# Kernel optimization log

Measured on AMD Instinct MI355X. Metric: run time of the kernel, lower is better.

The kernel has to match this reference:

```python
import jax, jax.numpy as jnp
import numpy as np

BATCH = 2
SEQ = 2048
D_MODEL = 512
D_STATE = 16
D_CONV = 4
D_INNER = 2 * D_MODEL  # expand=2


def setup_inputs() -> dict:
    key = jax.random.key(0)
    ks = jax.random.split(key, 7)
    s = 0.02
    x = jax.random.normal(ks[0], (BATCH, SEQ, D_MODEL), jnp.float32)
    W_in = jax.random.normal(ks[1], (2 * D_INNER, D_MODEL), jnp.float32) * s
    conv_w = jax.random.normal(ks[2], (D_INNER, 1, D_CONV), jnp.float32) * s  # depthwise kernel
    conv_b = jnp.zeros((D_INNER,), jnp.float32)
    W_x = jax.random.normal(ks[3], (2 * D_STATE, D_INNER), jnp.float32) * s
    W_dt = jax.random.normal(ks[4], (D_INNER, D_INNER), jnp.float32) * s
    b_dt = jnp.zeros((D_INNER,), jnp.float32)
    # A_log init: log of [1..d_state] broadcast over d_inner rows
    A_log = jnp.log(jnp.broadcast_to(jnp.arange(1, D_STATE + 1, dtype=jnp.float32), (D_INNER, D_STATE)))
    D_param = jnp.ones((D_INNER,), jnp.float32)
    W_out = jax.random.normal(ks[5], (D_MODEL, D_INNER), jnp.float32) * s
    return dict(x=x, W_in=W_in, conv_w=conv_w, conv_b=conv_b, W_x=W_x,
                W_dt=W_dt, b_dt=b_dt, A_log=A_log, D_param=D_param, W_out=W_out)


def reference(x, W_in, conv_w, conv_b, W_x, W_dt, b_dt, A_log, D_param, W_out):
    # in_proj, split into x-branch and gate z
    xz = x @ W_in.T                             # [B, L, 2*di]
    xi, z = jnp.split(xz, 2, axis=-1)
    # depthwise causal conv1d (torch pads both sides then slices [:seq_len] == left-pad only)
    h = jnp.transpose(xi, (0, 2, 1))            # [B, di, L]
    h = jax.lax.conv_general_dilated(
        h, conv_w, window_strides=(1,), padding=[(D_CONV - 1, 0)],
        dimension_numbers=('NCH', 'OIH', 'NCH'), feature_group_count=D_INNER)
    h = h + conv_b[None, :, None]
    h = jax.nn.silu(jnp.transpose(h, (0, 2, 1)))  # [B, L, di]

    A = -jnp.exp(A_log)                         # [di, ds]
    x_dbl = h @ W_x.T                           # [B, L, 2*ds]
    _delta_unused, Bmat = jnp.split(x_dbl, 2, axis=-1)  # B (also used as C): [B, L, ds]
    delta = jax.nn.softplus(h @ W_dt.T + b_dt)  # [B, L, di] (overwrites x_proj delta, as in source)

    def step(state, inp):
        d_t, B_t, h_t = inp                     # [B,di], [B,ds], [B,di]
        dA = jnp.exp(d_t[:, :, None] * A)       # [B, di, ds]
        state = dA * state + d_t[:, :, None] * B_t[:, None, :] * h_t[:, :, None]
        y_t = jnp.einsum('bds,bs->bd', state, B_t)  # C == B
        return state, y_t

    init = jnp.zeros((x.shape[0], D_INNER, D_STATE), x.dtype)
    _, ys = jax.lax.scan(step, init,
                         (jnp.swapaxes(delta, 0, 1), jnp.swapaxes(Bmat, 0, 1), jnp.swapaxes(h, 0, 1)))
    y = jnp.swapaxes(ys, 0, 1)                  # [B, L, di]
    y = (y + D_param * h) * jax.nn.silu(z)
    return y @ W_out.T                          # [B, L, d_model]
```

## Files before the change

### kernel.cpp

```cpp
#include <hip/hip_runtime.h>
#include <cstddef>
#include <cstdint>

#define NB 2
#define L_SEQ 2048
#define DM 512
#define DS 16
#define DI 1024
#define NC 64
#define CL (L_SEQ/NC)

typedef __attribute__((ext_vector_type(4))) float f32x4;
typedef __attribute__((ext_vector_type(8))) short bf16x8;

__device__ __forceinline__ float softplus_f(float x) {
  return (x > 20.f) ? x : log1pf(expf(x));
}
__device__ __forceinline__ float silu_f(float x) {
  return x / (1.f + expf(-x));
}
__device__ __forceinline__ ushort f2bf(float f) {
  uint32_t u = __float_as_uint(f);
  return (ushort)((u + 0x7fffu + ((u >> 16) & 1u)) >> 16);
}
__device__ __forceinline__ float bf2f(ushort h) {
  return __uint_as_float(((uint32_t)h) << 16);
}

__device__ __forceinline__ void gload16(const void* g, ushort* lds_wave_base) {
  __builtin_amdgcn_global_load_lds(
      (const __attribute__((address_space(1))) void*)g,
      (__attribute__((address_space(3))) void*)lds_wave_base, 16, 0, 0);
}

__global__ __launch_bounds__(256) void split_bf16(
    const float* __restrict__ in, ushort* __restrict__ hi,
    ushort* __restrict__ lo, int n4) {
  int i = blockIdx.x * 256 + threadIdx.x;
  if (i >= n4) return;
  float4 v = ((const float4*)in)[i];
  ushort h0 = f2bf(v.x), h1 = f2bf(v.y), h2 = f2bf(v.z), h3 = f2bf(v.w);
  ((ushort4*)hi)[i] = make_ushort4(h0, h1, h2, h3);
  ((ushort4*)lo)[i] = make_ushort4(
      f2bf(v.x - bf2f(h0)), f2bf(v.y - bf2f(h1)),
      f2bf(v.z - bf2f(h2)), f2bf(v.w - bf2f(h3)));
}

template <int ACT>
__global__ __launch_bounds__(512, 6) void gemm_mfma8(
    const ushort* __restrict__ Ahi, const ushort* __restrict__ Alo, int lda,
    const ushort* __restrict__ Bhi, const ushort* __restrict__ Blo, int ldb,
    const float* __restrict__ bias, float* __restrict__ C, int ldc,
    float* __restrict__ Bmout, int K) {
  constexpr int BM = 128, BN = 64;
  constexpr int AT = BM * 32;
  constexpr int BT = BN * 32;
  constexpr int BUF = 2 * AT + 2 * BT;
  constexpr int MR = 2, NR = 2;
  __shared__ __align__(16) ushort lds[2 * BUF];

  const int tid = threadIdx.x;
  const int lane = tid & 63;
  const int wave = tid >> 6;
  const int wr = wave >> 1;
  const int wc = wave & 1;

  const int nx = gridDim.x;
  const int nwg = nx * gridDim.y;
  int bid = blockIdx.y * nx + blockIdx.x;
  bid = (bid & 7) * (nwg >> 3) + (bid >> 3);
  const int m0 = (bid / nx) * BM;
  const int n0 = (bid % nx) * BN;

  const int ra = tid >> 2;
  const int kga = (tid & 3) ^ ((ra >> 1) & 3);
  const size_t aoff = (size_t)(m0 + ra) * lda + kga * 8;
  const int tq = tid & 255;
  const int rb = tq >> 2;
  const int kgb = (tq & 3) ^ ((rb >> 1) & 3);
  const size_t boff = (size_t)(n0 + rb) * ldb + kgb * 8;
  const ushort* Bsel = (wave < 4) ? Bhi : Blo;
  const int blds = 2 * AT + ((wave < 4) ? wave * 512 : BT + (wave - 4) * 512);

  const int fr = lane & 15, fq = lane >> 4;
  const int kswz = fq ^ ((fr >> 1) & 3);
  int aoffs[MR], boffs[NR];
#pragma unroll
  for (int m = 0; m < MR; m++) aoffs[m] = (wr * 32 + m * 16 + fr) * 32 + kswz * 8;
#pragma unroll
  for (int n = 0; n < NR; n++) boffs[n] = (wc * 32 + n * 16 + fr) * 32 + kswz * 8;

  f32x4 acc[MR][NR];
#pragma unroll
  for (int m = 0; m < MR; m++)
#pragma unroll
    for (int n = 0; n < NR; n++) acc[m][n] = (f32x4){0.f, 0.f, 0.f, 0.f};

  const int nsteps = K >> 5;

#define STAGE(base, kk)                                     \
  {                                                         \
    ushort* bp = (base);                                    \
    gload16(Ahi + aoff + (kk), bp + wave * 512);            \
    gload16(Alo + aoff + (kk), bp + AT + wave * 512);       \
    gload16(Bsel + boff + (kk), bp + blds);                 \
  }

#define COMPUTE(base)                                                          \
  {                                                                            \
    const ushort* cp = (base);                                                 \
    bf16x8 ah[MR], al[MR], bh[NR], bl[NR];                                     \
    _Pragma("unroll")                                                          \
    for (int m = 0; m < MR; m++) ah[m] = *(const bf16x8*)(cp + aoffs[m]);      \
    _Pragma("unroll")                                                          \
    for (int m = 0; m < MR; m++) al[m] = *(const bf16x8*)(cp + AT + aoffs[m]); \
    _Pragma("unroll")                                                          \
    for (int n = 0; n < NR; n++) bh[n] = *(const bf16x8*)(cp + 2 * AT + boffs[n]); \
    _Pragma("unroll")                                                          \
    for (int n = 0; n < NR; n++) bl[n] = *(const bf16x8*)(cp + 2 * AT + BT + boffs[n]); \
    _Pragma("unroll")                                                          \
    for (int m = 0; m < MR; m++)                                               \
      _Pragma("unroll")                                                        \
      for (int n = 0; n < NR; n++)                                             \
        acc[m][n] = __builtin_amdgcn_mfma_f32_16x16x32_bf16(ah[m], bh[n], acc[m][n], 0, 0, 0); \
    _Pragma("unroll")                                                          \
    for (int m = 0; m < MR; m++)                                               \
      _Pragma("unroll")                                                        \
      for (int n = 0; n < NR; n++)                                             \
        acc[m][n] = __builtin_amdgcn_mfma_f32_16x16x32_bf16(al[m], bh[n], acc[m][n], 0, 0, 0); \
    _Pragma("unroll")                                                          \
    for (int m = 0; m < MR; m++)                                               \
      _Pragma("unroll")                                                        \
      for (int n = 0; n < NR; n++)                                             \
        acc[m][n] = __builtin_amdgcn_mfma_f32_16x16x32_bf16(ah[m], bl[n], acc[m][n], 0, 0, 0); \
  }

  STAGE(lds, 0);
  __syncthreads();
  for (int t = 0; t < nsteps; ++t) {
    if (t + 1 < nsteps) STAGE(lds + ((t + 1) & 1) * BUF, (t + 1) << 5);
    COMPUTE(lds + (t & 1) * BUF);
    __syncthreads();
  }
#undef STAGE
#undef COMPUTE

#pragma unroll
  for (int m = 0; m < MR; m++) {
    const int row = m0 + wr * 32 + m * 16 + fq * 4;
#pragma unroll
    for (int n = 0; n < NR; n++) {
      const int col = n0 + wc * 32 + n * 16 + fr;
      if (ACT == 1) {
        if (col < DI) {
          const float bcol = bias[col];
#pragma unroll
          for (int j = 0; j < 4; j++)
            C[(size_t)(row + j) * ldc + col] = softplus_f(acc[m][n][j] + bcol);
        } else if (col < DI + DS) {
#pragma unroll
          for (int j = 0; j < 4; j++)
            Bmout[(size_t)(row + j) * DS + (col - DI)] = acc[m][n][j];
        }
      } else {
#pragma unroll
        for (int j = 0; j < 4; j++)
          C[(size_t)(row + j) * ldc + col] = acc[m][n][j];
      }
    }
  }
}

template <int ACT>
__global__ __launch_bounds__(256, 5) void gemm_mfma4(
    const ushort* __restrict__ Ahi, const ushort* __restrict__ Alo, int lda,
    const ushort* __restrict__ Bhi, const ushort* __restrict__ Blo, int ldb,
    const float* __restrict__ bias, float* __restrict__ C, int ldc, int K) {
  constexpr int BM = 64, BN = 64;
  constexpr int AT = BM * 32;
  constexpr int BT = BN * 32;
  constexpr int BUF = 2 * AT + 2 * BT;
  constexpr int MR = 2, NR = 2;
  __shared__ __align__(16) ushort lds[2 * BUF];

  const int tid = threadIdx.x;
  const int lane = tid & 63;
  const int wave = tid >> 6;
  const int wr = wave >> 1, wc = wave & 1;

  const int nx = gridDim.x;
  const int nwg = nx * gridDim.y;
  int bid = blockIdx.y * nx + blockIdx.x;
  bid = (bid & 7) * (nwg >> 3) + (bid >> 3);
  const int m0 = (bid / nx) * BM;
  const int n0 = (bid % nx) * BN;

  const int r0 = tid >> 2;
  const int kg = (tid & 3) ^ ((r0 >> 1) & 3);
  const size_t aoff0 = (size_t)(m0 + r0) * lda + kg * 8;
  const size_t boff0 = (size_t)(n0 + r0) * ldb + kg * 8;

  const int fr = lane & 15, fq = lane >> 4;
  const int kswz = fq ^ ((fr >> 1) & 3);
  int aoffs[MR], boffs[NR];
#pragma unroll
  for (int m = 0; m < MR; m++) aoffs[m] = (wr * 32 + m * 16 + fr) * 32 + kswz * 8;
#pragma unroll
  for (int n = 0; n < NR; n++) boffs[n] = (wc * 32 + n * 16 + fr) * 32 + kswz * 8;

  f32x4 acc[MR][NR];
#pragma unroll
  for (int m = 0; m < MR; m++)
#pragma unroll
    for (int n = 0; n < NR; n++) acc[m][n] = (f32x4){0.f, 0.f, 0.f, 0.f};

  const int nsteps = K >> 5;

#define STAGE(base, kk)                                           \
  {                                                               \
    ushort* bp = (base);                                          \
    gload16(Ahi + aoff0 + (kk), bp + wave * 512);                 \
    gload16(Alo + aoff0 + (kk), bp + AT + wave * 512);            \
    gload16(Bhi + boff0 + (kk), bp + 2 * AT + wave * 512);        \
    gload16(Blo + boff0 + (kk), bp + 2 * AT + BT + wave * 512);   \
  }

#define COMPUTE(base)                                                          \
  {                                                                            \
    const ushort* cp = (base);                                                 \
    bf16x8 ah[MR], al[MR], bh[NR], bl[NR];                                     \
    _Pragma("unroll")                                                          \
    for (int m = 0; m < MR; m++) ah[m] = *(const bf16x8*)(cp + aoffs[m]);      \
    _Pragma("unroll")                                                          \
    for (int m = 0; m < MR; m++) al[m] = *(const bf16x8*)(cp + AT + aoffs[m]); \
    _Pragma("unroll")                                                          \
    for (int n = 0; n < NR; n++) bh[n] = *(const bf16x8*)(cp + 2 * AT + boffs[n]); \
    _Pragma("unroll")                                                          \
    for (int n = 0; n < NR; n++) bl[n] = *(const bf16x8*)(cp + 2 * AT + BT + boffs[n]); \
    _Pragma("unroll")                                                          \
    for (int m = 0; m < MR; m++)                                               \
      _Pragma("unroll")                                                        \
      for (int n = 0; n < NR; n++)                                             \
        acc[m][n] = __builtin_amdgcn_mfma_f32_16x16x32_bf16(ah[m], bh[n], acc[m][n], 0, 0, 0); \
    _Pragma("unroll")                                                          \
    for (int m = 0; m < MR; m++)                                               \
      _Pragma("unroll")                                                        \
      for (int n = 0; n < NR; n++)                                             \
        acc[m][n] = __builtin_amdgcn_mfma_f32_16x16x32_bf16(al[m], bh[n], acc[m][n], 0, 0, 0); \
    _Pragma("unroll")                                                          \
    for (int m = 0; m < MR; m++)                                               \
      _Pragma("unroll")                                                        \
      for (int n = 0; n < NR; n++)                                             \
        acc[m][n] = __builtin_amdgcn_mfma_f32_16x16x32_bf16(ah[m], bl[n], acc[m][n], 0, 0, 0); \
  }

  STAGE(lds, 0);
  __syncthreads();
  for (int t = 0; t < nsteps; ++t) {
    if (t + 1 < nsteps) STAGE(lds + ((t + 1) & 1) * BUF, (t + 1) << 5);
    COMPUTE(lds + (t & 1) * BUF);
    __syncthreads();
  }
#undef STAGE
#undef COMPUTE

#pragma unroll
  for (int m = 0; m < MR; m++) {
    const int row = m0 + wr * 32 + m * 16 + fq * 4;
#pragma unroll
    for (int n = 0; n < NR; n++) {
      const int col = n0 + wc * 32 + n * 16 + fr;
      float bcol = (ACT == 1) ? bias[col] : 0.f;
#pragma unroll
      for (int j = 0; j < 4; j++) {
        float v = acc[m][n][j];
        if (ACT == 1) v = softplus_f(v + bcol);
        C[(size_t)(row + j) * ldc + col] = v;
      }
    }
  }
}

__global__ __launch_bounds__(256) void conv_silu_kernel(
    const float* __restrict__ xz, const float* __restrict__ conv_w,
    const float* __restrict__ conv_b, float* __restrict__ h,
    ushort* __restrict__ h_hi, ushort* __restrict__ h_lo) {
  const int idx = blockIdx.x * 256 + threadIdx.x;
  const int c = idx & (DI - 1);
  const int r = idx >> 10;
  const int l = r & (L_SEQ - 1);
  const float w0 = conv_w[c * 4 + 0];
  const float w1 = conv_w[c * 4 + 1];
  const float w2 = conv_w[c * 4 + 2];
  const float w3 = conv_w[c * 4 + 3];
  const float* xp = xz + (size_t)r * (2 * DI) + c;
  float acc = conv_b[c];
  if (l >= 3) acc += xp[-3 * 2 * DI] * w0;
  if (l >= 2) acc += xp[-2 * 2 * DI] * w1;
  if (l >= 1) acc += xp[-1 * 2 * DI] * w2;
  acc += xp[0] * w3;
  const float hv = silu_f(acc);
  h[idx] = hv;
  const ushort hh = f2bf(hv);
  h_hi[idx] = hh;
  h_lo[idx] = f2bf(hv - bf2f(hh));
}

__global__ __launch_bounds__(256) void scan_phase1(
    const float* __restrict__ delta, const float* __restrict__ h,
    const float* __restrict__ Bm, const float* __restrict__ A_log,
    float* __restrict__ aprod, float* __restrict__ blocal) {
  __shared__ float sB[CL * DS];
  const int tid = threadIdx.x;
  const int bid = blockIdx.x;
  const int cblk = bid & 3;
  const int chunk = (bid >> 2) & (NC - 1);
  const int b = bid >> 8;
  const int c = cblk * 256 + tid;
  const size_t row0 = (size_t)b * L_SEQ + chunk * CL;
  ((float2*)sB)[tid] = ((const float2*)(Bm + row0 * DS))[tid];
  __syncthreads();

  float Acs[DS], state[DS];
#pragma unroll
  for (int s = 0; s < DS; s += 4) {
    float4 al = *(const float4*)(A_log + (size_t)c * DS + s);
    Acs[s + 0] = -__expf(al.x);
    Acs[s + 1] = -__expf(al.y);
    Acs[s + 2] = -__expf(al.z);
    Acs[s + 3] = -__expf(al.w);
    state[s + 0] = 0.f; state[s + 1] = 0.f; state[s + 2] = 0.f; state[s + 3] = 0.f;
  }
  const float* dp = delta + row0 * DI + c;
  const float* hp = h + row0 * DI + c;
  float sdt = 0.f;
  for (int t = 0; t < CL; ++t) {
    const float dt = dp[(size_t)t * DI];
    const float ht = hp[(size_t)t * DI];
    const float dth = dt * ht;
    sdt += dt;
#pragma unroll
    for (int s = 0; s < DS; ++s)
      state[s] = __expf(dt * Acs[s]) * state[s] + dth * sB[t * DS + s];
  }
  const size_t o = (((size_t)b * NC + chunk) * DI + c) * DS;
#pragma unroll
  for (int s = 0; s < DS; s += 4) {
    *(float4*)(aprod + o + s) = make_float4(
        __expf(Acs[s] * sdt), __expf(Acs[s + 1] * sdt),
        __expf(Acs[s + 2] * sdt), __expf(Acs[s + 3] * sdt));
    *(float4*)(blocal + o + s) = make_float4(state[s], state[s + 1], state[s + 2], state[s + 3]);
  }
}

__global__ __launch_bounds__(256) void scan_phase2(
    float* __restrict__ aprod, const float* __restrict__ blocal) {
  const int idx = blockIdx.x * 256 + threadIdx.x;
  const int b = idx >> 14;
  const int cs = idx & 16383;
  float st = 0.f;
  for (int ch = 0; ch < NC; ++ch) {
    const size_t o = (size_t)(b * NC + ch) * (DI * DS) + cs;
    const float a = aprod[o];
    const float bl = blocal[o];
    aprod[o] = st;
    st = a * st + bl;
  }
}

__global__ __launch_bounds__(256) void scan_phase3(
    const float* __restrict__ delta, const float* __restrict__ h,
    const float* __restrict__ Bm, const float* __restrict__ A_log,
    const float* __restrict__ sinit, float* __restrict__ xz,
    const float* __restrict__ Dp) {
  __shared__ float sB[CL * DS];
  const int tid = threadIdx.x;
  const int bid = blockIdx.x;
  const int cblk = bid & 3;
  const int chunk = (bid >> 2) & (NC - 1);
  const int b = bid >> 8;
  const int c = cblk * 256 + tid;
  const size_t row0 = (size_t)b * L_SEQ + chunk * CL;
  ((float2*)sB)[tid] = ((const float2*)(Bm + row0 * DS))[tid];
  __syncthreads();

  float Acs[DS], state[DS];
  const size_t o = (((size_t)b * NC + chunk) * DI + c) * DS;
#pragma unroll
  for (int s = 0; s < DS; s += 4) {
    float4 al = *(const float4*)(A_log + (size_t)c * DS + s);
    Acs[s + 0] = -__expf(al.x);
    Acs[s + 1] = -__expf(al.y);
    Acs[s + 2] = -__expf(al.z);
    Acs[s + 3] = -__expf(al.w);
    float4 sv = *(const float4*)(sinit + o + s);
    state[s + 0] = sv.x; state[s + 1] = sv.y; state[s + 2] = sv.z; state[s + 3] = sv.w;
  }
  const float* dp = delta + row0 * DI + c;
  const float* hp = h + row0 * DI + c;
  const float* zp = xz + row0 * (2 * DI) + DI + c;
  ushort* yrow = (ushort*)(xz + row0 * (2 * DI)) + c;
  const float Dc = Dp[c];
  for (int t = 0; t < CL; ++t) {
    const float dt = dp[(size_t)t * DI];
    const float ht = hp[(size_t)t * DI];
    const float z = zp[(size_t)t * (2 * DI)];
    const float dth = dt * ht;
    float yv = 0.f;
#pragma unroll
    for (int s = 0; s < DS; ++s) {
      const float bt = sB[t * DS + s];
      state[s] = __expf(dt * Acs[s]) * state[s] + dth * bt;
      yv += state[s] * bt;
    }
    const float g = (yv + Dc * ht) * silu_f(z);
    const ushort gh = f2bf(g);
    yrow[(size_t)t * 4096] = gh;
    yrow[(size_t)t * 4096 + 1024] = f2bf(g - bf2f(gh));
  }
}

extern "C" void kernel_launch(void* const* d_in, const int* in_sizes, int n_in,
                              void* d_out, int out_size, void* d_ws, size_t ws_size,
                              hipStream_t stream) {
  const float* x      = (const float*)d_in[0];
  const float* W_in   = (const float*)d_in[1];
  const float* conv_w = (const float*)d_in[2];
  const float* conv_b = (const float*)d_in[3];
  const float* W_x    = (const float*)d_in[4];
  const float* W_dt   = (const float*)d_in[5];
  const float* b_dt   = (const float*)d_in[6];
  const float* A_log  = (const float*)d_in[7];
  const float* D_par  = (const float*)d_in[8];
  const float* W_out  = (const float*)d_in[9];
  float* out = (float*)d_out;

  const int rows = NB * L_SEQ;

  float* xz     = (float*)d_ws;
  float* h      = xz + (size_t)(8u << 20);
  float* delta  = h + (size_t)(4u << 20);
  float* Bm     = delta + (size_t)(4u << 20);
  ushort* W2hi  = (ushort*)(Bm + (size_t)(64u << 10));
  ushort* W2lo  = W2hi + (size_t)1088 * 1024;
  ushort* Wout_hi = W2lo + (size_t)1088 * 1024;
  ushort* Wout_lo = Wout_hi + (size_t)(512u << 10);
  float* xreg   = (float*)(Wout_lo + (size_t)(512u << 10));
  ushort* x_hi  = (ushort*)xreg;
  ushort* x_lo  = x_hi + (size_t)(2u << 20);
  ushort* Win_hi = x_lo + (size_t)(2u << 20);
  ushort* Win_lo = Win_hi + (size_t)(1u << 20);
  ushort* h_hi  = (ushort*)xreg;
  ushort* h_lo  = h_hi + (size_t)(4u << 20);
  float* aprod  = xreg;
  float* blocal = aprod + (size_t)(2u << 20);
  ushort* y_hi  = (ushort*)xz;
  ushort* y_lo  = y_hi + 1024;

  split_bf16<<<2048, 256, 0, stream>>>(x, x_hi, x_lo, rows * DM / 4);
  split_bf16<<<1024, 256, 0, stream>>>(W_in, Win_hi, Win_lo, 2 * DI * DM / 4);
  split_bf16<<<1024, 256, 0, stream>>>(W_dt, W2hi, W2lo, DI * DI / 4);
  split_bf16<<<16, 256, 0, stream>>>(W_x + DS * DI,
      W2hi + (size_t)DI * DI, W2lo + (size_t)DI * DI, DS * DI / 4);
  split_bf16<<<512, 256, 0, stream>>>(W_out, Wout_hi, Wout_lo, DM * DI / 4);

  gemm_mfma8<0><<<dim3(32, 32), 512, 0, stream>>>(
      x_hi, x_lo, DM, Win_hi, Win_lo, DM, nullptr, xz, 2 * DI, nullptr, DM);
  conv_silu_kernel<<<(rows * DI) / 256, 256, 0, stream>>>(xz, conv_w, conv_b, h, h_hi, h_lo);
  gemm_mfma8<1><<<dim3(17, 32), 512, 0, stream>>>(
      h_hi, h_lo, DI, W2hi, W2lo, DI, b_dt, delta, DI, Bm, DI);
  scan_phase1<<<NB * NC * (DI / 256), 256, 0, stream>>>(delta, h, Bm, A_log, aprod, blocal);
  scan_phase2<<<(NB * DI * DS) / 256, 256, 0, stream>>>(aprod, blocal);
  scan_phase3<<<NB * NC * (DI / 256), 256, 0, stream>>>(delta, h, Bm, A_log, aprod, xz, D_par);
  gemm_mfma4<0><<<dim3(8, 64), 256, 0, stream>>>(
      y_hi, y_lo, 4096, Wout_hi, Wout_lo, DI, nullptr, out, DM, DI);
}
```

Measured before the change: 208.6 us.

## Triple-buffer GEMM LDS pipeline with split barriers and fuse bf16 split launches

New measurement: 201.7 us. 3.3% less time.

```diff
diff --git a/kernel.cpp b/kernel.cpp
--- a/kernel.cpp
+++ b/kernel.cpp
@@ -33,21 +33,37 @@
       (__attribute__((address_space(3))) void*)lds_wave_base, 16, 0, 0);
 }
 
-__global__ __launch_bounds__(256) void split_bf16(
-    const float* __restrict__ in, ushort* __restrict__ hi,
-    ushort* __restrict__ lo, int n4) {
-  int i = blockIdx.x * 256 + threadIdx.x;
-  if (i >= n4) return;
+__device__ __forceinline__ void split4(const float4 v, ushort4* hi, ushort4* lo) {
+  ushort h0 = f2bf(v.x), h1 = f2bf(v.y), h2 = f2bf(v.z), h3 = f2bf(v.w);
+  *hi = make_ushort4(h0, h1, h2, h3);
+  *lo = make_ushort4(f2bf(v.x - bf2f(h0)), f2bf(v.y - bf2f(h1)),
+                     f2bf(v.z - bf2f(h2)), f2bf(v.w - bf2f(h3)));
+}
+
+__global__ __launch_bounds__(256) void split_all(
+    const float* __restrict__ x,    ushort* __restrict__ xh,  ushort* __restrict__ xl,
+    const float* __restrict__ win,  ushort* __restrict__ wih, ushort* __restrict__ wil,
+    const float* __restrict__ wdt,  ushort* __restrict__ wdh, ushort* __restrict__ wdl,
+    const float* __restrict__ wx,   ushort* __restrict__ wxh, ushort* __restrict__ wxl,
+    const float* __restrict__ wout, ushort* __restrict__ woh, ushort* __restrict__ wol) {
+  int bi = blockIdx.x;
+  const float* in; ushort* hi; ushort* lo; int i;
+  if (bi < 2048)      { in = x;    hi = xh;  lo = xl;  i = bi * 256 + threadIdx.x; }
+  else if (bi < 3072) { in = win;  hi = wih; lo = wil; i = (bi - 2048) * 256 + threadIdx.x; }
+  else if (bi < 4096) { in = wdt;  hi = wdh; lo = wdl; i = (bi - 3072) * 256 + threadIdx.x; }
+  else if (bi < 4112) { in = wx;   hi = wxh; lo = wxl; i = (bi - 4096) * 256 + threadIdx.x; }
+  else                { in = wout; hi = woh; lo = wol; i = (bi - 4112) * 256 + threadIdx.x; }
   float4 v = ((const float4*)in)[i];
-  ushort h0 = f2bf(v.x), h1 = f2bf(v.y), h2 = f2bf(v.z), h3 = f2bf(v.w);
-  ((ushort4*)hi)[i] = make_ushort4(h0, h1, h2, h3);
-  ((ushort4*)lo)[i] = make_ushort4(
-      f2bf(v.x - bf2f(h0)), f2bf(v.y - bf2f(h1)),
-      f2bf(v.z - bf2f(h2)), f2bf(v.w - bf2f(h3)));
-}
+  ushort4 h4, l4;
+  split4(v, &h4, &l4);
+  ((ushort4*)hi)[i] = h4;
+  ((ushort4*)lo)[i] = l4;
+}
+
+#define MFMA(a, b, c) __builtin_amdgcn_mfma_f32_16x16x32_bf16((a), (b), (c), 0, 0, 0)
 
 template <int ACT>
-__global__ __launch_bounds__(512, 6) void gemm_mfma8(
+__global__ __launch_bounds__(512, 4) void gemm_mfma8(
     const ushort* __restrict__ Ahi, const ushort* __restrict__ Alo, int lda,
     const ushort* __restrict__ Bhi, const ushort* __restrict__ Blo, int ldb,
     const float* __restrict__ bias, float* __restrict__ C, int ldc,
@@ -56,8 +72,7 @@
   constexpr int AT = BM * 32;
   constexpr int BT = BN * 32;
   constexpr int BUF = 2 * AT + 2 * BT;
-  constexpr int MR = 2, NR = 2;
-  __shared__ __align__(16) ushort lds[2 * BUF];
+  __shared__ __align__(16) ushort lds[3 * BUF];
 
   const int tid = threadIdx.x;
   const int lane = tid & 63;
@@ -84,72 +99,81 @@
 
   const int fr = lane & 15, fq = lane >> 4;
   const int kswz = fq ^ ((fr >> 1) & 3);
-  int aoffs[MR], boffs[NR];
-#pragma unroll
-  for (int m = 0; m < MR; m++) aoffs[m] = (wr * 32 + m * 16 + fr) * 32 + kswz * 8;
-#pragma unroll
-  for (int n = 0; n < NR; n++) boffs[n] = (wc * 32 + n * 16 + fr) * 32 + kswz * 8;
-
-  f32x4 acc[MR][NR];
-#pragma unroll
-  for (int m = 0; m < MR; m++)
-#pragma unroll
-    for (int n = 0; n < NR; n++) acc[m][n] = (f32x4){0.f, 0.f, 0.f, 0.f};
+  int aoffs[2], boffs[2];
+#pragma unroll
+  for (int m = 0; m < 2; m++) aoffs[m] = (wr * 32 + m * 16 + fr) * 32 + kswz * 8;
+#pragma unroll
+  for (int n = 0; n < 2; n++) boffs[n] = (wc * 32 + n * 16 + fr) * 32 + kswz * 8;
+
+  f32x4 acc[2][2];
+#pragma unroll
+  for (int m = 0; m < 2; m++)
+#pragma unroll
+    for (int n = 0; n < 2; n++) acc[m][n] = (f32x4){0.f, 0.f, 0.f, 0.f};
 
   const int nsteps = K >> 5;
 
-#define STAGE(base, kk)                                     \
-  {                                                         \
-    ushort* bp = (base);                                    \
-    gload16(Ahi + aoff + (kk), bp + wave * 512);            \
-    gload16(Alo + aoff + (kk), bp + AT + wave * 512);       \
-    gload16(Bsel + boff + (kk), bp + blds);                 \
-  }
-
-#define COMPUTE(base)                                                          \
-  {                                                                            \
-    const ushort* cp = (base);                                                 \
-    bf16x8 ah[MR], al[MR], bh[NR], bl[NR];                                     \
-    _Pragma("unroll")                                                          \
-    for (int m = 0; m < MR; m++) ah[m] = *(const bf16x8*)(cp + aoffs[m]);      \
-    _Pragma("unroll")                                                          \
-    for (int m = 0; m < MR; m++) al[m] = *(const bf16x8*)(cp + AT + aoffs[m]); \
-    _Pragma("unroll")                                                          \
-    for (int n = 0; n < NR; n++) bh[n] = *(const bf16x8*)(cp + 2 * AT + boffs[n]); \
-    _Pragma("unroll")                                                          \
-    for (int n = 0; n < NR; n++) bl[n] = *(const bf16x8*)(cp + 2 * AT + BT + boffs[n]); \
-    _Pragma("unroll")                                                          \
-    for (int m = 0; m < MR; m++)                                               \
-      _Pragma("unroll")                                                        \
-      for (int n = 0; n < NR; n++)                                             \
-        acc[m][n] = __builtin_amdgcn_mfma_f32_16x16x32_bf16(ah[m], bh[n], acc[m][n], 0, 0, 0); \
-    _Pragma("unroll")                                                          \
-    for (int m = 0; m < MR; m++)                                               \
-      _Pragma("unroll")                                                        \
-      for (int n = 0; n < NR; n++)                                             \
-        acc[m][n] = __builtin_amdgcn_mfma_f32_16x16x32_bf16(al[m], bh[n], acc[m][n], 0, 0, 0); \
-    _Pragma("unroll")                                                          \
-    for (int m = 0; m < MR; m++)                                               \
-      _Pragma("unroll")                                                        \
-      for (int n = 0; n < NR; n++)                                             \
-        acc[m][n] = __builtin_amdgcn_mfma_f32_16x16x32_bf16(ah[m], bl[n], acc[m][n], 0, 0, 0); \
-  }
-
-  STAGE(lds, 0);
-  __syncthreads();
+  gload16(Ahi + aoff + 0, lds + wave * 512);
+  gload16(Alo + aoff + 0, lds + AT + wave * 512);
+  gload16(Bsel + boff + 0, lds + blds);
+  gload16(Ahi + aoff + 32, lds + BUF + wave * 512);
+  gload16(Alo + aoff + 32, lds + BUF + AT + wave * 512);
+  gload16(Bsel + boff + 32, lds + BUF + blds);
+
+  int cur = 0;
   for (int t = 0; t < nsteps; ++t) {
-    if (t + 1 < nsteps) STAGE(lds + ((t + 1) & 1) * BUF, (t + 1) << 5);
-    COMPUTE(lds + (t & 1) * BUF);
-    __syncthreads();
-  }
-#undef STAGE
-#undef COMPUTE
-
-#pragma unroll
-  for (int m = 0; m < MR; m++) {
+    const ushort* cp = lds + cur * BUF;
+    const int nxt = (cur + 2) % 3;
+    ushort* np = lds + nxt * BUF;
+    const bool pf = (t + 2) < nsteps;
+    const int kk2 = (t + 2) << 5;
+    if (t + 1 < nsteps) asm volatile("s_waitcnt vmcnt(3)" ::: "memory");
+    else                asm volatile("s_waitcnt vmcnt(0)" ::: "memory");
+    __builtin_amdgcn_s_barrier();
+    bf16x8 ah0 = *(const bf16x8*)(cp + aoffs[0]);
+    bf16x8 ah1 = *(const bf16x8*)(cp + aoffs[1]);
+    bf16x8 bh0 = *(const bf16x8*)(cp + 2 * AT + boffs[0]);
+    bf16x8 bh1 = *(const bf16x8*)(cp + 2 * AT + boffs[1]);
+    __builtin_amdgcn_sched_barrier(0);
+    __builtin_amdgcn_s_setprio(1);
+    acc[0][0] = MFMA(ah0, bh0, acc[0][0]);
+    acc[0][1] = MFMA(ah0, bh1, acc[0][1]);
+    acc[1][0] = MFMA(ah1, bh0, acc[1][0]);
+    acc[1][1] = MFMA(ah1, bh1, acc[1][1]);
+    __builtin_amdgcn_s_setprio(0);
+    __builtin_amdgcn_s_barrier();
+    bf16x8 al0 = *(const bf16x8*)(cp + AT + aoffs[0]);
+    bf16x8 al1 = *(const bf16x8*)(cp + AT + aoffs[1]);
+    if (pf) {
+      gload16(Ahi + aoff + kk2, np + wave * 512);
+      gload16(Alo + aoff + kk2, np + AT + wave * 512);
+    }
+    __builtin_amdgcn_sched_barrier(0);
+    __builtin_amdgcn_s_setprio(1);
+    acc[0][0] = MFMA(al0, bh0, acc[0][0]);
+    acc[0][1] = MFMA(al0, bh1, acc[0][1]);
+    acc[1][0] = MFMA(al1, bh0, acc[1][0]);
+    acc[1][1] = MFMA(al1, bh1, acc[1][1]);
+    __builtin_amdgcn_s_setprio(0);
+    __builtin_amdgcn_s_barrier();
+    bf16x8 bl0 = *(const bf16x8*)(cp + 2 * AT + BT + boffs[0]);
+    bf16x8 bl1 = *(const bf16x8*)(cp + 2 * AT + BT + boffs[1]);
+    if (pf) gload16(Bsel + boff + kk2, np + blds);
+    __builtin_amdgcn_sched_barrier(0);
+    __builtin_amdgcn_s_setprio(1);
+    acc[0][0] = MFMA(ah0, bl0, acc[0][0]);
+    acc[0][1] = MFMA(ah0, bl1, acc[0][1]);
+    acc[1][0] = MFMA(ah1, bl0, acc[1][0]);
+    acc[1][1] = MFMA(ah1, bl1, acc[1][1]);
+    __builtin_amdgcn_s_setprio(0);
+    cur = (cur + 1) % 3;
+  }
+
+#pragma unroll
+  for (int m = 0; m < 2; m++) {
     const int row = m0 + wr * 32 + m * 16 + fq * 4;
 #pragma unroll
-    for (int n = 0; n < NR; n++) {
+    for (int n = 0; n < 2; n++) {
       const int col = n0 + wc * 32 + n * 16 + fr;
       if (ACT == 1) {
         if (col < DI) {
@@ -171,17 +195,15 @@
   }
 }
 
-template <int ACT>
-__global__ __launch_bounds__(256, 5) void gemm_mfma4(
+__global__ __launch_bounds__(256, 6) void gemm_mfma4(
     const ushort* __restrict__ Ahi, const ushort* __restrict__ Alo, int lda,
     const ushort* __restrict__ Bhi, const ushort* __restrict__ Blo, int ldb,
-    const float* __restrict__ bias, float* __restrict__ C, int ldc, int K) {
+    float* __restrict__ C, int ldc, int K) {
   constexpr int BM = 64, BN = 64;
   constexpr int AT = BM * 32;
   constexpr int BT = BN * 32;
   constexpr int BUF = 2 * AT + 2 * BT;
-  constexpr int MR = 2, NR = 2;
-  __shared__ __align__(16) ushort lds[2 * BUF];
+  __shared__ __align__(16) ushort lds[3 * BUF];
 
   const int tid = threadIdx.x;
   const int lane = tid & 63;
@@ -197,86 +219,98 @@
 
   const int r0 = tid >> 2;
   const int kg = (tid & 3) ^ ((r0 >> 1) & 3);
-  const size_t aoff0 = (size_t)(m0 + r0) * lda + kg * 8;
-  const size_t boff0 = (size_t)(n0 + r0) * ldb + kg * 8;
+  const size_t aoff = (size_t)(m0 + r0) * lda + kg * 8;
+  const size_t boff = (size_t)(n0 + r0) * ldb + kg * 8;
 
   const int fr = lane & 15, fq = lane >> 4;
   const int kswz = fq ^ ((fr >> 1) & 3);
-  int aoffs[MR], boffs[NR];
-#pragma unroll
-  for (int m = 0; m < MR; m++) aoffs[m] = (wr * 32 + m * 16 + fr) * 32 + kswz * 8;
-#pragma unroll
-  for (int n = 0; n < NR; n++) boffs[n] = (wc * 32 + n * 16 + fr) * 32 + kswz * 8;
-
-  f32x4 acc[MR][NR];
-#pragma unroll
-  for (int m = 0; m < MR; m++)
-#pragma unroll
-    for (int n = 0; n < NR; n++) acc[m][n] = (f32x4){0.f, 0.f, 0.f, 0.f};
+  int aoffs[2], boffs[2];
+#pragma unroll
+  for (int m = 0; m < 2; m++) aoffs[m] = (wr * 32 + m * 16 + fr) * 32 + kswz * 8;
+#pragma unroll
+  for (int n = 0; n < 2; n++) boffs[n] = (wc * 32 + n * 16 + fr) * 32 + kswz * 8;
+
+  f32x4 acc[2][2];
+#pragma unroll
+  for (int m = 0; m < 2; m++)
+#pragma unroll
+    for (int n = 0; n < 2; n++) acc[m][n] = (f32x4){0.f, 0.f, 0.f, 0.f};
 
   const int nsteps = K >> 5;
 
-#define STAGE(base, kk)                                           \
-  {                                                               \
-    ushort* bp = (base);                                          \
-    gload16(Ahi + aoff0 + (kk), bp + wave * 512);                 \
-    gload16(Alo + aoff0 + (kk), bp + AT + wave * 512);            \
-    gload16(Bhi + boff0 + (kk), bp + 2 * AT + wave * 512);        \
-    gload16(Blo + boff0 + (kk), bp + 2 * AT + BT + wave * 512);   \
-  }
-
-#define COMPUTE(base)                                                          \
-  {                                                                            \
-    const ushort* cp = (base);                                                 \
-    bf16x8 ah[MR], al[MR], bh[NR], bl[NR];                                     \
-    _Pragma("unroll")                                                          \
-    for (int m = 0; m < MR; m++) ah[m] = *(const bf16x8*)(cp + aoffs[m]);      \
-    _Pragma("unroll")                                                          \
-    for (int m = 0; m < MR; m++) al[m] = *(const bf16x8*)(cp + AT + aoffs[m]); \
-    _Pragma("unroll")                                                          \
-    for (int n = 0; n < NR; n++) bh[n] = *(const bf16x8*)(cp + 2 * AT + boffs[n]); \
-    _Pragma("unroll")                                                          \
-    for (int n = 0; n < NR; n++) bl[n] = *(const bf16x8*)(cp + 2 * AT + BT + boffs[n]); \
-    _Pragma("unroll")                                                          \
-    for (int m = 0; m < MR; m++)                                               \
-      _Pragma("unroll")                                                        \
-      for (int n = 0; n < NR; n++)                                             \
-        acc[m][n] = __builtin_amdgcn_mfma_f32_16x16x32_bf16(ah[m], bh[n], acc[m][n], 0, 0, 0); \
-    _Pragma("unroll")                                                          \
-    for (int m = 0; m < MR; m++)                                               \
-      _Pragma("unroll")                                                        \
-      for (int n = 0; n < NR; n++)                                             \
-        acc[m][n] = __builtin_amdgcn_mfma_f32_16x16x32_bf16(al[m], bh[n], acc[m][n], 0, 0, 0); \
-    _Pragma("unroll")                                                          \
-    for (int m = 0; m < MR; m++)                                               \
-      _Pragma("unroll")                                                        \
-      for (int n = 0; n < NR; n++)                                             \
-        acc[m][n] = __builtin_amdgcn_mfma_f32_16x16x32_bf16(ah[m], bl[n], acc[m][n], 0, 0, 0); \
-  }
-
-  STAGE(lds, 0);
-  __syncthreads();
+#define STAGE4(bufi, kk)                                              \
+  {                                                                   \
+    ushort* bp = lds + (bufi) * BUF;                                  \
+    gload16(Ahi + aoff + (kk), bp + wave * 512);                      \
+    gload16(Alo + aoff + (kk), bp + AT + wave * 512);                 \
+    gload16(Bhi + boff + (kk), bp + 2 * AT + wave * 512);             \
+    gload16(Blo + boff + (kk), bp + 2 * AT + BT + wave * 512);        \
+  }
+
+  STAGE4(0, 0);
+  STAGE4(1, 32);
+  int cur = 0;
   for (int t = 0; t < nsteps; ++t) {
-    if (t + 1 < nsteps) STAGE(lds + ((t + 1) & 1) * BUF, (t + 1) << 5);
-    COMPUTE(lds + (t & 1) * BUF);
-    __syncthreads();
-  }
-#undef STAGE
-#undef COMPUTE
-
-#pragma unroll
-  for (int m = 0; m < MR; m++) {
+    const ushort* cp = lds + cur * BUF;
+    const int nxt = (cur + 2) % 3;
+    ushort* np = lds + nxt * BUF;
+    const bool pf = (t + 2) < nsteps;
+    const int kk2 = (t + 2) << 5;
+    if (t + 1 < nsteps) asm volatile("s_waitcnt vmcnt(4)" ::: "memory");
+    else                asm volatile("s_waitcnt vmcnt(0)" ::: "memory");
+    __builtin_amdgcn_s_barrier();
+    bf16x8 ah0 = *(const bf16x8*)(cp + aoffs[0]);
+    bf16x8 ah1 = *(const bf16x8*)(cp + aoffs[1]);
+    bf16x8 bh0 = *(const bf16x8*)(cp + 2 * AT + boffs[0]);
+    bf16x8 bh1 = *(const bf16x8*)(cp + 2 * AT + boffs[1]);
+    __builtin_amdgcn_sched_barrier(0);
+    __builtin_amdgcn_s_setprio(1);
+    acc[0][0] = MFMA(ah0, bh0, acc[0][0]);
+    acc[0][1] = MFMA(ah0, bh1, acc[0][1]);
+    acc[1][0] = MFMA(ah1, bh0, acc[1][0]);
+    acc[1][1] = MFMA(ah1, bh1, acc[1][1]);
+    __builtin_amdgcn_s_setprio(0);
+    __builtin_amdgcn_s_barrier();
+    bf16x8 al0 = *(const bf16x8*)(cp + AT + aoffs[0]);
+    bf16x8 al1 = *(const bf16x8*)(cp + AT + aoffs[1]);
+    if (pf) {
+      gload16(Ahi + aoff + kk2, np + wave * 512);
+      gload16(Alo + aoff + kk2, np + AT + wave * 512);
+    }
+    __builtin_amdgcn_sched_barrier(0);
+    __builtin_amdgcn_s_setprio(1);
+    acc[0][0] = MFMA(al0, bh0, acc[0][0]);
+    acc[0][1] = MFMA(al0, bh1, acc[0][1]);
+    acc[1][0] = MFMA(al1, bh0, acc[1][0]);
+    acc[1][1] = MFMA(al1, bh1, acc[1][1]);
+    __builtin_amdgcn_s_setprio(0);
+    __builtin_amdgcn_s_barrier();
+    bf16x8 bl0 = *(const bf16x8*)(cp + 2 * AT + BT + boffs[0]);
+    bf16x8 bl1 = *(const bf16x8*)(cp + 2 * AT + BT + boffs[1]);
+    if (pf) {
+      gload16(Bhi + boff + kk2, np + 2 * AT + wave * 512);
+      gload16(Blo + boff + kk2, np + 2 * AT + BT + wave * 512);
+    }
+    __builtin_amdgcn_sched_barrier(0);
+    __builtin_amdgcn_s_setprio(1);
+    acc[0][0] = MFMA(ah0, bl0, acc[0][0]);
+    acc[0][1] = MFMA(ah0, bl1, acc[0][1]);
+    acc[1][0] = MFMA(ah1, bl0, acc[1][0]);
+    acc[1][1] = MFMA(ah1, bl1, acc[1][1]);
+    __builtin_amdgcn_s_setprio(0);
+    cur = (cur + 1) % 3;
+  }
+#undef STAGE4
+
+#pragma unroll
+  for (int m = 0; m < 2; m++) {
     const int row = m0 + wr * 32 + m * 16 + fq * 4;
 #pragma unroll
-    for (int n = 0; n < NR; n++) {
+    for (int n = 0; n < 2; n++) {
       const int col = n0 + wc * 32 + n * 16 + fr;
-      float bcol = (ACT == 1) ? bias[col] : 0.f;
-#pragma unroll
-      for (int j = 0; j < 4; j++) {
-        float v = acc[m][n][j];
-        if (ACT == 1) v = softplus_f(v + bcol);
-        C[(size_t)(row + j) * ldc + col] = v;
-      }
+#pragma unroll
+      for (int j = 0; j < 4; j++)
+        C[(size_t)(row + j) * ldc + col] = acc[m][n][j];
     }
   }
 }
@@ -435,8 +469,6 @@
   const float* W_out  = (const float*)d_in[9];
   float* out = (float*)d_out;
 
-  const int rows = NB * L_SEQ;
-
   float* xz     = (float*)d_ws;
   float* h      = xz + (size_t)(8u << 20);
   float* delta  = h + (size_t)(4u << 20);
@@ -457,12 +489,12 @@
   ushort* y_hi  = (ushort*)xz;
   ushort* y_lo  = y_hi + 1024;
 
-  split_bf16<<<2048, 256, 0, stream>>>(x, x_hi, x_lo, rows * DM / 4);
-  split_bf16<<<1024, 256, 0, stream>>>(W_in, Win_hi, Win_lo, 2 * DI * DM / 4);
-  split_bf16<<<1024, 256, 0, stream>>>(W_dt, W2hi, W2lo, DI * DI / 4);
-  split_bf16<<<16, 256, 0, stream>>>(W_x + DS * DI,
-      W2hi + (size_t)DI * DI, W2lo + (size_t)DI * DI, DS * DI / 4);
-  split_bf16<<<512, 256, 0, stream>>>(W_out, Wout_hi, Wout_lo, DM * DI / 4);
+  const int rows = NB * L_SEQ;
+
+  split_all<<<4624, 256, 0, stream>>>(
+      x, x_hi, x_lo, W_in, Win_hi, Win_lo, W_dt, W2hi, W2lo,
+      W_x + DS * DI, W2hi + (size_t)DI * DI, W2lo + (size_t)DI * DI,
+      W_out, Wout_hi, Wout_lo);
 
   gemm_mfma8<0><<<dim3(32, 32), 512, 0, stream>>>(
       x_hi, x_lo, DM, Win_hi, Win_lo, DM, nullptr, xz, 2 * DI, nullptr, DM);
@@ -472,6 +504,6 @@
   scan_phase1<<<NB * NC * (DI / 256), 256, 0, stream>>>(delta, h, Bm, A_log, aprod, blocal);
   scan_phase2<<<(NB * DI * DS) / 256, 256, 0, stream>>>(aprod, blocal);
   scan_phase3<<<NB * NC * (DI / 256), 256, 0, stream>>>(delta, h, Bm, A_log, aprod, xz, D_par);
-  gemm_mfma4<0><<<dim3(8, 64), 256, 0, stream>>>(
-      y_hi, y_lo, 4096, Wout_hi, Wout_lo, DI, nullptr, out, DM, DI);
-}
+  gemm_mfma4<<<dim3(8, 64), 256, 0, stream>>>(
+      y_hi, y_lo, 4096, Wout_hi, Wout_lo, DI, out, DM, DI);
+}
```

## Triple-buffer GEMM LDS pipeline with vmcnt waits and fuse split launches

Applied to the files above, without the earlier changes.

Result: faster. 200.7 us, median of 2 (-3.8%).

```diff
diff --git a/kernel.cpp b/kernel.cpp
--- a/kernel.cpp
+++ b/kernel.cpp
@@ -33,21 +33,37 @@
       (__attribute__((address_space(3))) void*)lds_wave_base, 16, 0, 0);
 }
 
-__global__ __launch_bounds__(256) void split_bf16(
-    const float* __restrict__ in, ushort* __restrict__ hi,
-    ushort* __restrict__ lo, int n4) {
-  int i = blockIdx.x * 256 + threadIdx.x;
-  if (i >= n4) return;
+__device__ __forceinline__ void split4(const float4 v, ushort4* hi, ushort4* lo) {
+  ushort h0 = f2bf(v.x), h1 = f2bf(v.y), h2 = f2bf(v.z), h3 = f2bf(v.w);
+  *hi = make_ushort4(h0, h1, h2, h3);
+  *lo = make_ushort4(f2bf(v.x - bf2f(h0)), f2bf(v.y - bf2f(h1)),
+                     f2bf(v.z - bf2f(h2)), f2bf(v.w - bf2f(h3)));
+}
+
+__global__ __launch_bounds__(256) void split_all(
+    const float* __restrict__ x,    ushort* __restrict__ xh,  ushort* __restrict__ xl,
+    const float* __restrict__ win,  ushort* __restrict__ wih, ushort* __restrict__ wil,
+    const float* __restrict__ wdt,  ushort* __restrict__ wdh, ushort* __restrict__ wdl,
+    const float* __restrict__ wx,   ushort* __restrict__ wxh, ushort* __restrict__ wxl,
+    const float* __restrict__ wout, ushort* __restrict__ woh, ushort* __restrict__ wol) {
+  int bi = blockIdx.x;
+  const float* in; ushort* hi; ushort* lo; int i;
+  if (bi < 2048)      { in = x;    hi = xh;  lo = xl;  i = bi * 256 + threadIdx.x; }
+  else if (bi < 3072) { in = win;  hi = wih; lo = wil; i = (bi - 2048) * 256 + threadIdx.x; }
+  else if (bi < 4096) { in = wdt;  hi = wdh; lo = wdl; i = (bi - 3072) * 256 + threadIdx.x; }
+  else if (bi < 4112) { in = wx;   hi = wxh; lo = wxl; i = (bi - 4096) * 256 + threadIdx.x; }
+  else                { in = wout; hi = woh; lo = wol; i = (bi - 4112) * 256 + threadIdx.x; }
   float4 v = ((const float4*)in)[i];
-  ushort h0 = f2bf(v.x), h1 = f2bf(v.y), h2 = f2bf(v.z), h3 = f2bf(v.w);
-  ((ushort4*)hi)[i] = make_ushort4(h0, h1, h2, h3);
-  ((ushort4*)lo)[i] = make_ushort4(
-      f2bf(v.x - bf2f(h0)), f2bf(v.y - bf2f(h1)),
-      f2bf(v.z - bf2f(h2)), f2bf(v.w - bf2f(h3)));
-}
+  ushort4 h4, l4;
+  split4(v, &h4, &l4);
+  ((ushort4*)hi)[i] = h4;
+  ((ushort4*)lo)[i] = l4;
+}
+
+#define MFMA(a, b, c) __builtin_amdgcn_mfma_f32_16x16x32_bf16((a), (b), (c), 0, 0, 0)
 
 template <int ACT>
-__global__ __launch_bounds__(512, 6) void gemm_mfma8(
+__global__ __launch_bounds__(512, 4) void gemm_mfma8(
     const ushort* __restrict__ Ahi, const ushort* __restrict__ Alo, int lda,
     const ushort* __restrict__ Bhi, const ushort* __restrict__ Blo, int ldb,
     const float* __restrict__ bias, float* __restrict__ C, int ldc,
@@ -57,7 +73,7 @@
   constexpr int BT = BN * 32;
   constexpr int BUF = 2 * AT + 2 * BT;
   constexpr int MR = 2, NR = 2;
-  __shared__ __align__(16) ushort lds[2 * BUF];
+  __shared__ __align__(16) ushort lds[3 * BUF];
 
   const int tid = threadIdx.x;
   const int lane = tid & 63;
@@ -122,25 +138,29 @@
     for (int m = 0; m < MR; m++)                                               \
       _Pragma("unroll")                                                        \
       for (int n = 0; n < NR; n++)                                             \
-        acc[m][n] = __builtin_amdgcn_mfma_f32_16x16x32_bf16(ah[m], bh[n], acc[m][n], 0, 0, 0); \
-    _Pragma("unroll")                                                          \
-    for (int m = 0; m < MR; m++)                                               \
-      _Pragma("unroll")                                                        \
-      for (int n = 0; n < NR; n++)                                             \
-        acc[m][n] = __builtin_amdgcn_mfma_f32_16x16x32_bf16(al[m], bh[n], acc[m][n], 0, 0, 0); \
-    _Pragma("unroll")                                                          \
-    for (int m = 0; m < MR; m++)                                               \
-      _Pragma("unroll")                                                        \
-      for (int n = 0; n < NR; n++)                                             \
-        acc[m][n] = __builtin_amdgcn_mfma_f32_16x16x32_bf16(ah[m], bl[n], acc[m][n], 0, 0, 0); \
+        acc[m][n] = MFMA(ah[m], bh[n], acc[m][n]);                             \
+    _Pragma("unroll")                                                          \
+    for (int m = 0; m < MR; m++)                                               \
+      _Pragma("unroll")                                                        \
+      for (int n = 0; n < NR; n++)                                             \
+        acc[m][n] = MFMA(al[m], bh[n], acc[m][n]);                             \
+    _Pragma("unroll")                                                          \
+    for (int m = 0; m < MR; m++)                                               \
+      _Pragma("unroll")                                                        \
+      for (int n = 0; n < NR; n++)                                             \
+        acc[m][n] = MFMA(ah[m], bl[n], acc[m][n]);                             \
   }
 
   STAGE(lds, 0);
-  __syncthreads();
+  STAGE(lds + BUF, 32);
+  int ocur = 0, onext = BUF, ofar = 2 * BUF;
   for (int t = 0; t < nsteps; ++t) {
-    if (t + 1 < nsteps) STAGE(lds + ((t + 1) & 1) * BUF, (t + 1) << 5);
-    COMPUTE(lds + (t & 1) * BUF);
-    __syncthreads();
+    if (t == nsteps - 1) asm volatile("s_waitcnt vmcnt(0)" ::: "memory");
+    else                 asm volatile("s_waitcnt vmcnt(3)" ::: "memory");
+    __builtin_amdgcn_s_barrier();
+    if (t + 2 < nsteps) STAGE(lds + ofar, (t + 2) << 5);
+    COMPUTE(lds + ocur);
+    int tmp = ocur; ocur = onext; onext = ofar; ofar = tmp;
   }
 #undef STAGE
 #undef COMPUTE
@@ -171,17 +191,16 @@
   }
 }
 
-template <int ACT>
-__global__ __launch_bounds__(256, 5) void gemm_mfma4(
+__global__ __launch_bounds__(256, 3) void gemm_mfma4(
     const ushort* __restrict__ Ahi, const ushort* __restrict__ Alo, int lda,
     const ushort* __restrict__ Bhi, const ushort* __restrict__ Blo, int ldb,
-    const float* __restrict__ bias, float* __restrict__ C, int ldc, int K) {
+    float* __restrict__ C, int ldc, int K) {
   constexpr int BM = 64, BN = 64;
   constexpr int AT = BM * 32;
   constexpr int BT = BN * 32;
   constexpr int BUF = 2 * AT + 2 * BT;
   constexpr int MR = 2, NR = 2;
-  __shared__ __align__(16) ushort lds[2 * BUF];
+  __shared__ __align__(16) ushort lds[3 * BUF];
 
   const int tid = threadIdx.x;
   const int lane = tid & 63;
@@ -197,8 +216,8 @@
 
   const int r0 = tid >> 2;
   const int kg = (tid & 3) ^ ((r0 >> 1) & 3);
-  const size_t aoff0 = (size_t)(m0 + r0) * lda + kg * 8;
-  const size_t boff0 = (size_t)(n0 + r0) * ldb + kg * 8;
+  const size_t aoff = (size_t)(m0 + r0) * lda + kg * 8;
+  const size_t boff = (size_t)(n0 + r0) * ldb + kg * 8;
 
   const int fr = lane & 15, fq = lane >> 4;
   const int kswz = fq ^ ((fr >> 1) & 3);
@@ -216,16 +235,16 @@
 
   const int nsteps = K >> 5;
 
-#define STAGE(base, kk)                                           \
+#define STAGE4(base, kk)                                          \
   {                                                               \
     ushort* bp = (base);                                          \
-    gload16(Ahi + aoff0 + (kk), bp + wave * 512);                 \
-    gload16(Alo + aoff0 + (kk), bp + AT + wave * 512);            \
-    gload16(Bhi + boff0 + (kk), bp + 2 * AT + wave * 512);        \
-    gload16(Blo + boff0 + (kk), bp + 2 * AT + BT + wave * 512);   \
-  }
-
-#define COMPUTE(base)                                                          \
+    gload16(Ahi + aoff + (kk), bp + wave * 512);                  \
+    gload16(Alo + aoff + (kk), bp + AT + wave * 512);             \
+    gload16(Bhi + boff + (kk), bp + 2 * AT + wave * 512);         \
+    gload16(Blo + boff + (kk), bp + 2 * AT + BT + wave * 512);    \
+  }
+
+#define COMPUTE4(base)                                                         \
   {                                                                            \
     const ushort* cp = (base);                                                 \
     bf16x8 ah[MR], al[MR], bh[NR], bl[NR];                                     \
@@ -241,28 +260,32 @@
     for (int m = 0; m < MR; m++)                                               \
       _Pragma("unroll")                                                        \
       for (int n = 0; n < NR; n++)                                             \
-        acc[m][n] = __builtin_amdgcn_mfma_f32_16x16x32_bf16(ah[m], bh[n], acc[m][n], 0, 0, 0); \
-    _Pragma("unroll")                                                          \
-    for (int m = 0; m < MR; m++)                                               \
-      _Pragma("unroll")                                                        \
-      for (int n = 0; n < NR; n++)                                             \
-        acc[m][n] = __builtin_amdgcn_mfma_f32_16x16x32_bf16(al[m], bh[n], acc[m][n], 0, 0, 0); \
-    _Pragma("unroll")                                                          \
-    for (int m = 0; m < MR; m++)                                               \
-      _Pragma("unroll")                                                        \
-      for (int n = 0; n < NR; n++)                                             \
-        acc[m][n] = __builtin_amdgcn_mfma_f32_16x16x32_bf16(ah[m], bl[n], acc[m][n], 0, 0, 0); \
-  }
-
-  STAGE(lds, 0);
-  __syncthreads();
+        acc[m][n] = MFMA(ah[m], bh[n], acc[m][n]);                             \
+    _Pragma("unroll")                                                          \
+    for (int m = 0; m < MR; m++)                                               \
+      _Pragma("unroll")                                                        \
+      for (int n = 0; n < NR; n++)                                             \
+        acc[m][n] = MFMA(al[m], bh[n], acc[m][n]);                             \
+    _Pragma("unroll")                                                          \
+    for (int m = 0; m < MR; m++)                                               \
+      _Pragma("unroll")                                                        \
+      for (int n = 0; n < NR; n++)                                             \
+        acc[m][n] = MFMA(ah[m], bl[n], acc[m][n]);                             \
+  }
+
+  STAGE4(lds, 0);
+  STAGE4(lds + BUF, 32);
+  int ocur = 0, onext = BUF, ofar = 2 * BUF;
   for (int t = 0; t < nsteps; ++t) {
-    if (t + 1 < nsteps) STAGE(lds + ((t + 1) & 1) * BUF, (t + 1) << 5);
-    COMPUTE(lds + (t & 1) * BUF);
-    __syncthreads();
-  }
-#undef STAGE
-#undef COMPUTE
+    if (t == nsteps - 1) asm volatile("s_waitcnt vmcnt(0)" ::: "memory");
+    else                 asm volatile("s_waitcnt vmcnt(4)" ::: "memory");
+    __builtin_amdgcn_s_barrier();
+    if (t + 2 < nsteps) STAGE4(lds + ofar, (t + 2) << 5);
+    COMPUTE4(lds + ocur);
+    int tmp = ocur; ocur = onext; onext = ofar; ofar = tmp;
+  }
+#undef STAGE4
+#undef COMPUTE4
 
 #pragma unroll
   for (int m = 0; m < MR; m++) {
@@ -270,13 +293,9 @@
 #pragma unroll
     for (int n = 0; n < NR; n++) {
       const int col = n0 + wc * 32 + n * 16 + fr;
-      float bcol = (ACT == 1) ? bias[col] : 0.f;
-#pragma unroll
-      for (int j = 0; j < 4; j++) {
-        float v = acc[m][n][j];
-        if (ACT == 1) v = softplus_f(v + bcol);
-        C[(size_t)(row + j) * ldc + col] = v;
-      }
+#pragma unroll
+      for (int j = 0; j < 4; j++)
+        C[(size_t)(row + j) * ldc + col] = acc[m][n][j];
     }
   }
 }
@@ -435,8 +454,6 @@
   const float* W_out  = (const float*)d_in[9];
   float* out = (float*)d_out;
 
-  const int rows = NB * L_SEQ;
-
   float* xz     = (float*)d_ws;
   float* h      = xz + (size_t)(8u << 20);
   float* delta  = h + (size_t)(4u << 20);
@@ -457,12 +474,12 @@
   ushort* y_hi  = (ushort*)xz;
   ushort* y_lo  = y_hi + 1024;
 
-  split_bf16<<<2048, 256, 0, stream>>>(x, x_hi, x_lo, rows * DM / 4);
-  split_bf16<<<1024, 256, 0, stream>>>(W_in, Win_hi, Win_lo, 2 * DI * DM / 4);
-  split_bf16<<<1024, 256, 0, stream>>>(W_dt, W2hi, W2lo, DI * DI / 4);
-  split_bf16<<<16, 256, 0, stream>>>(W_x + DS * DI,
-      W2hi + (size_t)DI * DI, W2lo + (size_t)DI * DI, DS * DI / 4);
-  split_bf16<<<512, 256, 0, stream>>>(W_out, Wout_hi, Wout_lo, DM * DI / 4);
+  const int rows = NB * L_SEQ;
+
+  split_all<<<4624, 256, 0, stream>>>(
+      x, x_hi, x_lo, W_in, Win_hi, Win_lo, W_dt, W2hi, W2lo,
+      W_x + DS * DI, W2hi + (size_t)DI * DI, W2lo + (size_t)DI * DI,
+      W_out, Wout_hi, Wout_lo);
 
   gemm_mfma8<0><<<dim3(32, 32), 512, 0, stream>>>(
       x_hi, x_lo, DM, Win_hi, Win_lo, DM, nullptr, xz, 2 * DI, nullptr, DM);
@@ -472,6 +489,6 @@
   scan_phase1<<<NB * NC * (DI / 256), 256, 0, stream>>>(delta, h, Bm, A_log, aprod, blocal);
   scan_phase2<<<(NB * DI * DS) / 256, 256, 0, stream>>>(aprod, blocal);
   scan_phase3<<<NB * NC * (DI / 256), 256, 0, stream>>>(delta, h, Bm, A_log, aprod, xz, D_par);
-  gemm_mfma4<0><<<dim3(8, 64), 256, 0, stream>>>(
-      y_hi, y_lo, 4096, Wout_hi, Wout_lo, DI, nullptr, out, DM, DI);
-}
+  gemm_mfma4<<<dim3(8, 64), 256, 0, stream>>>(
+      y_hi, y_lo, 4096, Wout_hi, Wout_lo, DI, out, DM, DI);
+}
```
